# Performance work log

Measured on AMD Instinct MI355X. Metric: run time of the kernel, lower is better.

## Reference

```python
import jax, jax.numpy as jnp
import numpy as np

N = 50000
E = 800000
IN, HID, OUT = 256, 128, 64
NEG_SLOPE = 0.2


def _gat(x, src, dst, W, a_src, a_dst, b, heads, dim, concat):
    # PyG GATConv (eval mode, self-loops already appended to src/dst)
    xh = (x @ W).reshape(N, heads, dim)              # [N,H,D]
    s_src = jnp.einsum('nhd,hd->nh', xh, a_src)       # [N,H]
    s_dst = jnp.einsum('nhd,hd->nh', xh, a_dst)
    e = jax.nn.leaky_relu(s_src[src] + s_dst[dst], NEG_SLOPE)  # [Etot,H]
    m = jax.ops.segment_max(e, dst, num_segments=N)
    e = jnp.exp(e - m[dst])
    z = jax.ops.segment_sum(e, dst, num_segments=N)
    alpha = e / z[dst]                                # segment softmax over incoming edges
    msg = xh[src] * alpha[:, :, None]                 # [Etot,H,D] gather + weight
    out = jax.ops.segment_sum(msg, dst, num_segments=N)  # scatter-add aggregate
    out = out.reshape(N, heads * dim) if concat else out.mean(axis=1)
    return out + b


def setup_inputs():
    key = jax.random.key(0)
    ks = jax.random.split(key, 20)
    sc = 0.05
    inp = {
        'x': jax.random.normal(ks[0], (N, IN), jnp.float32),
        'edge_index': jax.random.randint(ks[1], (2, E), 0, N, jnp.int64) if jax.config.read('jax_enable_x64') else jax.random.randint(ks[1], (2, E), 0, N, jnp.int32),
        # semantic MLP
        'w1': jax.random.normal(ks[2], (IN, HID), jnp.float32) * sc,
        'b1': jnp.zeros((HID,), jnp.float32),
        'w2': jax.random.normal(ks[3], (HID, HID), jnp.float32) * sc,
        'b2': jnp.zeros((HID,), jnp.float32),
        # gat1: HID -> HID//2, heads=4, concat -> 2*HID
        'g1_w': jax.random.normal(ks[4], (HID, 4 * (HID // 2)), jnp.float32) * sc,
        'g1_asrc': jax.random.normal(ks[5], (4, HID // 2), jnp.float32) * sc,
        'g1_adst': jax.random.normal(ks[6], (4, HID // 2), jnp.float32) * sc,
        'g1_b': jnp.zeros((2 * HID,), jnp.float32),
        # gat2: 2*HID -> OUT, heads=2, mean
        'g2_w': jax.random.normal(ks[7], (2 * HID, 2 * OUT), jnp.float32) * sc,
        'g2_asrc': jax.random.normal(ks[8], (2, OUT), jnp.float32) * sc,
        'g2_adst': jax.random.normal(ks[9], (2, OUT), jnp.float32) * sc,
        'g2_b': jnp.zeros((OUT,), jnp.float32),
        # gat3: OUT -> OUT, heads=1, mean
        'g3_w': jax.random.normal(ks[10], (OUT, OUT), jnp.float32) * sc,
        'g3_asrc': jax.random.normal(ks[11], (1, OUT), jnp.float32) * sc,
        'g3_adst': jax.random.normal(ks[12], (1, OUT), jnp.float32) * sc,
        'g3_b': jnp.zeros((OUT,), jnp.float32),
    }
    return inp


def reference(x, edge_index, w1, b1, w2, b2,
              g1_w, g1_asrc, g1_adst, g1_b,
              g2_w, g2_asrc, g2_adst, g2_b,
              g3_w, g3_asrc, g3_adst, g3_b):
    # add self loops once (PyG GATConv default add_self_loops=True)
    loop = jnp.arange(N, dtype=edge_index.dtype)
    src = jnp.concatenate([edge_index[0], loop])
    dst = jnp.concatenate([edge_index[1], loop])
    # semantic MLP (eval: dropout is identity)
    h = jax.nn.relu(x @ w1 + b1)
    h = jax.nn.relu(h @ w2 + b2)
    h = jax.nn.elu(_gat(h, src, dst, g1_w, g1_asrc, g1_adst, g1_b, 4, HID // 2, True))
    h = jax.nn.elu(_gat(h, src, dst, g2_w, g2_asrc, g2_adst, g2_b, 2, OUT, False))
    h = _gat(h, src, dst, g3_w, g3_asrc, g3_adst, g3_b, 1, OUT, False)
    return h
```

## Files before the change

### kernel.cpp

```cpp
#include <hip/hip_runtime.h>
#include <hip/hip_fp16.h>
#include <math.h>

#define NN 50000
#define NE 800000

static inline int ceil_div_h(int a, int b) { return (a + b - 1) / b; }

typedef _Float16 half8 __attribute__((ext_vector_type(8)));
typedef float f32x4 __attribute__((ext_vector_type(4)));

__global__ __launch_bounds__(256)
void prep_kernel(const float* __restrict__ w1, const float* __restrict__ w2,
                 const float* __restrict__ g1w, const float* __restrict__ g2w,
                 const float* __restrict__ g3w, __half* __restrict__ wt,
                 int* __restrict__ cursor) {
  int idx = blockIdx.x * 256 + threadIdx.x;
  if (idx < NN) cursor[idx] = 0;
  const float* W; int K, N, li;
  if (idx < 32768)        { W = w1;  K = 256; N = 128; li = idx; }
  else if (idx < 49152)   { W = w2;  K = 128; N = 128; li = idx - 32768; }
  else if (idx < 81920)   { W = g1w; K = 128; N = 256; li = idx - 49152; }
  else if (idx < 114688)  { W = g2w; K = 256; N = 128; li = idx - 81920; }
  else if (idx < 118784)  { W = g3w; K = 64;  N = 64;  li = idx - 114688; }
  else return;
  int n = li / K, k = li - n * K;
  wt[idx] = __float2half_rn(W[(size_t)k * N + n]);
}

__global__ __launch_bounds__(256)
void mlp_gat1_fused(const float* __restrict__ x,
                    const __half* __restrict__ wt1,
                    const float* __restrict__ b1,
                    const __half* __restrict__ wt2,
                    const float* __restrict__ b2,
                    const __half* __restrict__ wtg1,
                    const float* __restrict__ a_src, const float* __restrict__ a_dst,
                    __half* __restrict__ xh1,
                    float* __restrict__ s_src, float* __restrict__ s_dst) {
  constexpr int SA = 40;
  constexpr int SH = 136;
  __shared__ __align__(16) _Float16 smem[25088];
  _Float16* As   = smem;
  _Float16* Bs12 = smem + 2560;
  _Float16* h1s  = smem + 7680;
  _Float16* h2s  = smem + 16384;
  _Float16* Bs3  = Bs12;
  const int tid = threadIdx.x;
  const int bm = blockIdx.x * 64;
  const int wave = tid >> 6, lane = tid & 63;
  const int l16 = lane & 15, quad = lane >> 4;
  const int wm = (wave & 1) * 32;
  const int wn = (wave >> 1) * 64;

  {
    f32x4 acc[2][4] = {};
    for (int k0 = 0; k0 < 256; k0 += 32) {
      #pragma unroll
      for (int i = 0; i < 2; ++i) {
        int idx = tid + i * 256;
        int m = idx >> 3, q = idx & 7;
        int gm = bm + m;
        float4 v = make_float4(0.f, 0.f, 0.f, 0.f);
        if (gm < NN) v = *(const float4*)&x[(size_t)gm * 256 + k0 + q * 4];
        union { __half2 h2[2]; float2 f2; } u;
        u.h2[0] = __floats2half2_rn(v.x, v.y);
        u.h2[1] = __floats2half2_rn(v.z, v.w);
        *(float2*)&As[m * SA + q * 4] = u.f2;
      }
      #pragma unroll
      for (int i = 0; i < 2; ++i) {
        int idx = tid + i * 256;
        int n = idx >> 2, kq = (idx & 3) * 8;
        *(float4*)&Bs12[n * SA + kq] = *(const float4*)&wt1[(size_t)n * 256 + k0 + kq];
      }
      __syncthreads();
      half8 af[2], bf[4];
      #pragma unroll
      for (int mi = 0; mi < 2; ++mi)
        af[mi] = *(const half8*)&As[(wm + mi * 16 + l16) * SA + quad * 8];
      #pragma unroll
      for (int ni = 0; ni < 4; ++ni)
        bf[ni] = *(const half8*)&Bs12[(wn + ni * 16 + l16) * SA + quad * 8];
      #pragma unroll
      for (int mi = 0; mi < 2; ++mi)
        #pragma unroll
        for (int ni = 0; ni < 4; ++ni)
          acc[mi][ni] = __builtin_amdgcn_mfma_f32_16x16x32_f16(af[mi], bf[ni], acc[mi][ni], 0, 0, 0);
      __syncthreads();
    }
    #pragma unroll
    for (int mi = 0; mi < 2; ++mi)
      #pragma unroll
      for (int r = 0; r < 4; ++r) {
        int row = wm + mi * 16 + quad * 4 + r;
        #pragma unroll
        for (int ni = 0; ni < 4; ++ni) {
          int col = wn + ni * 16 + l16;
          float v = acc[mi][ni][r] + b1[col];
          v = fmaxf(v, 0.f);
          h1s[row * SH + col] = (_Float16)v;
        }
      }
  }
  __syncthreads();

  {
    f32x4 acc[2][4] = {};
    for (int k0 = 0; k0 < 128; k0 += 32) {
      #pragma unroll
      for (int i = 0; i < 2; ++i) {
        int idx = tid + i * 256;
        int n = idx >> 2, kq = (idx & 3) * 8;
        *(float4*)&Bs12[n * SA + kq] = *(const float4*)&wt2[(size_t)n * 128 + k0 + kq];
      }
      __syncthreads();
      half8 af[2], bf[4];
      #pragma unroll
      for (int mi = 0; mi < 2; ++mi)
        af[mi] = *(const half8*)&h1s[(wm + mi * 16 + l16) * SH + k0 + quad * 8];
      #pragma unroll
      for (int ni = 0; ni < 4; ++ni)
        bf[ni] = *(const half8*)&Bs12[(wn + ni * 16 + l16) * SA + quad * 8];
      #pragma unroll
      for (int mi = 0; mi < 2; ++mi)
        #pragma unroll
        for (int ni = 0; ni < 4; ++ni)
          acc[mi][ni] = __builtin_amdgcn_mfma_f32_16x16x32_f16(af[mi], bf[ni], acc[mi][ni], 0, 0, 0);
      __syncthreads();
    }
    #pragma unroll
    for (int mi = 0; mi < 2; ++mi)
      #pragma unroll
      for (int r = 0; r < 4; ++r) {
        int row = wm + mi * 16 + quad * 4 + r;
        #pragma unroll
        for (int ni = 0; ni < 4; ++ni) {
          int col = wn + ni * 16 + l16;
          float v = acc[mi][ni][r] + b2[col];
          v = fmaxf(v, 0.f);
          h2s[row * SH + col] = (_Float16)v;
        }
      }
  }
  __syncthreads();

  {
    f32x4 acc[4][4] = {};
    const int wn3 = wave * 64;
    for (int k0 = 0; k0 < 128; k0 += 32) {
      #pragma unroll
      for (int i = 0; i < 4; ++i) {
        int idx = tid + i * 256;
        int n = idx >> 2, kq = (idx & 3) * 8;
        *(float4*)&Bs3[n * SA + kq] = *(const float4*)&wtg1[(size_t)n * 128 + k0 + kq];
      }
      __syncthreads();
      half8 af[4], bf[4];
      #pragma unroll
      for (int mi = 0; mi < 4; ++mi)
        af[mi] = *(const half8*)&h2s[(mi * 16 + l16) * SH + k0 + quad * 8];
      #pragma unroll
      for (int ni = 0; ni < 4; ++ni)
        bf[ni] = *(const half8*)&Bs3[(wn3 + ni * 16 + l16) * SA + quad * 8];
      #pragma unroll
      for (int mi = 0; mi < 4; ++mi)
        #pragma unroll
        for (int ni = 0; ni < 4; ++ni)
          acc[mi][ni] = __builtin_amdgcn_mfma_f32_16x16x32_f16(af[mi], bf[ni], acc[mi][ni], 0, 0, 0);
      __syncthreads();
    }
    float asv[4], adv[4];
    #pragma unroll
    for (int ni = 0; ni < 4; ++ni) {
      int d = ni * 16 + l16;
      asv[ni] = a_src[wave * 64 + d];
      adv[ni] = a_dst[wave * 64 + d];
    }
    #pragma unroll
    for (int mi = 0; mi < 4; ++mi) {
      #pragma unroll
      for (int r = 0; r < 4; ++r) {
        int gm = bm + mi * 16 + quad * 4 + r;
        float ss = 0.f, sd = 0.f;
        #pragma unroll
        for (int ni = 0; ni < 4; ++ni) {
          float v = acc[mi][ni][r];
          ss = fmaf(v, asv[ni], ss);
          sd = fmaf(v, adv[ni], sd);
          if (gm < NN) xh1[(size_t)gm * 256 + wn3 + ni * 16 + l16] = __float2half_rn(v);
        }
        #pragma unroll
        for (int off = 1; off < 16; off <<= 1) {
          ss += __shfl_xor(ss, off, 64);
          sd += __shfl_xor(sd, off, 64);
        }
        if (l16 == 0 && gm < NN) {
          s_src[gm * 4 + wave] = ss;
          s_dst[gm * 4 + wave] = sd;
        }
      }
    }
  }
}

template<int BM, int TN, int WR, int WC, int ACT, int OUTH, int AF32, int HS>
__global__ __launch_bounds__(256)
void mfma_gemm(const void* __restrict__ Av, const __half* __restrict__ Bt,
               const float* __restrict__ bias, void* __restrict__ Cv,
               const float* __restrict__ a_src, const float* __restrict__ a_dst,
               float* __restrict__ s_src, float* __restrict__ s_dst,
               int M, int N, int K) {
  constexpr int FM = BM / WR / 16;
  constexpr int FN = TN / WC / 16;
  constexpr int SA = 40;
  __shared__ __align__(16) _Float16 As[BM * SA];
  __shared__ __align__(16) _Float16 Bs[TN * SA];
  const int tid = threadIdx.x;
  const int bm = blockIdx.y * BM, bn = blockIdx.x * TN;
  const int wave = tid >> 6, lane = tid & 63;
  const int wm = (wave % WR) * (BM / WR);
  const int wn = (wave / WR) * (TN / WC);
  const int l16 = lane & 15, quad = lane >> 4;

  f32x4 acc[FM][FN] = {};

  for (int k0 = 0; k0 < K; k0 += 32) {
    if (AF32) {
      const float* A = (const float*)Av;
      #pragma unroll
      for (int i = 0; i < (BM * 8) / 256; ++i) {
        int idx = tid + i * 256;
        int m = idx >> 3, q = idx & 7;
        int gm = bm + m;
        float4 v = make_float4(0.f, 0.f, 0.f, 0.f);
        if (gm < M) v = *(const float4*)&A[(size_t)gm * K + k0 + q * 4];
        union { __half2 h2[2]; float2 f2; } u;
        u.h2[0] = __floats2half2_rn(v.x, v.y);
        u.h2[1] = __floats2half2_rn(v.z, v.w);
        *(float2*)&As[m * SA + q * 4] = u.f2;
      }
    } else {
      const __half* A = (const __half*)Av;
      #pragma unroll
      for (int i = 0; i < (BM * 4) / 256; ++i) {
        int idx = tid + i * 256;
        int m = idx >> 2, q = (idx & 3) * 8;
        int gm = bm + m;
        float4 raw = make_float4(0.f, 0.f, 0.f, 0.f);
        if (gm < M) raw = *(const float4*)&A[(size_t)gm * K + k0 + q];
        *(float4*)&As[m * SA + q] = raw;
      }
    }
    #pragma unroll
    for (int i = 0; i < (TN * 4) / 256; ++i) {
      int idx = tid + i * 256;
      int n = idx >> 2, kq = (idx & 3) * 8;
      float4 raw = *(const float4*)&Bt[(size_t)(bn + n) * K + k0 + kq];
      *(float4*)&Bs[n * SA + kq] = raw;
    }
    __syncthreads();
    half8 af[FM], bf[FN];
    #pragma unroll
    for (int mi = 0; mi < FM; ++mi)
      af[mi] = *(const half8*)&As[(wm + mi * 16 + l16) * SA + quad * 8];
    #pragma unroll
    for (int ni = 0; ni < FN; ++ni)
      bf[ni] = *(const half8*)&Bs[(wn + ni * 16 + l16) * SA + quad * 8];
    #pragma unroll
    for (int mi = 0; mi < FM; ++mi)
      #pragma unroll
      for (int ni = 0; ni < FN; ++ni)
        acc[mi][ni] = __builtin_amdgcn_mfma_f32_16x16x32_f16(af[mi], bf[ni], acc[mi][ni], 0, 0, 0);
    __syncthreads();
  }

  #pragma unroll
  for (int mi = 0; mi < FM; ++mi) {
    #pragma unroll
    for (int r = 0; r < 4; ++r) {
      int gm = bm + wm + mi * 16 + quad * 4 + r;
      if (gm >= M) continue;
      #pragma unroll
      for (int ni = 0; ni < FN; ++ni) {
        int gn = bn + wn + ni * 16 + l16;
        float v = acc[mi][ni][r];
        if (bias) v += bias[gn];
        if (ACT == 1) v = fmaxf(v, 0.f);
        if (OUTH) ((__half*)Cv)[(size_t)gm * N + gn] = __float2half_rn(v);
        else      ((float*)Cv)[(size_t)gm * N + gn] = v;
      }
    }
  }

  if (HS > 0) {
    const int h = (bn + wn) >> 6;
    float asv[FN], adv[FN];
    #pragma unroll
    for (int ni = 0; ni < FN; ++ni) {
      int d = ni * 16 + l16;
      asv[ni] = a_src[h * 64 + d];
      adv[ni] = a_dst[h * 64 + d];
    }
    #pragma unroll
    for (int mi = 0; mi < FM; ++mi) {
      #pragma unroll
      for (int r = 0; r < 4; ++r) {
        float ss = 0.f, sd = 0.f;
        #pragma unroll
        for (int ni = 0; ni < FN; ++ni) {
          float v = acc[mi][ni][r];
          ss = fmaf(v, asv[ni], ss);
          sd = fmaf(v, adv[ni], sd);
        }
        #pragma unroll
        for (int off = 1; off < 16; off <<= 1) {
          ss += __shfl_xor(ss, off, 64);
          sd += __shfl_xor(sd, off, 64);
        }
        int gm = bm + wm + mi * 16 + quad * 4 + r;
        if (l16 == 0 && gm < M) {
          s_src[gm * HS + h] = ss;
          s_dst[gm * HS + h] = sd;
        }
      }
    }
  }
}


__global__ __launch_bounds__(256)
void hist_kernel(const int* __restrict__ ei, int* __restrict__ cnt) {
  int e = blockIdx.x * blockDim.x + threadIdx.x;
  if (e >= NE) return;
  atomicAdd(&cnt[ei[NE + e]], 1);
}

__global__ __launch_bounds__(256)
void scan1_kernel(const int* __restrict__ in, int* __restrict__ out,
                  int* __restrict__ bsum, int n) {
  __shared__ int tmp[256];
  int t = threadIdx.x;
  int i = blockIdx.x * 256 + t;
  int v = (i < n) ? in[i] : 0;
  tmp[t] = v;
  __syncthreads();
  for (int off = 1; off < 256; off <<= 1) {
    int u = (t >= off) ? tmp[t - off] : 0;
    __syncthreads();
    tmp[t] += u;
    __syncthreads();
  }
  if (i <= n) out[i] = tmp[t] - v;
  if (t == 255) bsum[blockIdx.x] = tmp[255];
}

__global__ __launch_bounds__(256)
void scan3_kernel(int* __restrict__ out, const int* __restrict__ bsum,
                  int* __restrict__ cursor, int n, int nb) {
  __shared__ int tmp[256];
  int t = threadIdx.x;
  int bv = (t < nb) ? bsum[t] : 0;
  tmp[t] = bv;
  __syncthreads();
  for (int off = 1; off < 256; off <<= 1) {
    int u = (t >= off) ? tmp[t - off] : 0;
    __syncthreads();
    tmp[t] += u;
    __syncthreads();
  }
  int add = tmp[blockIdx.x] - ((blockIdx.x < nb) ? bsum[blockIdx.x] : 0);
  int i = blockIdx.x * 256 + t;
  if (i > n) return;
  int v = out[i] + add;
  out[i] = v;
  if (i < n) cursor[i] = v;
}

__global__ __launch_bounds__(256)
void scatter_kernel(const int* __restrict__ ei, int* __restrict__ cursor,
                    int* __restrict__ srcs) {
  int e = blockIdx.x * blockDim.x + threadIdx.x;
  if (e >= NE) return;
  int s = ei[e], d = ei[NE + e];
  int pos = atomicAdd(&cursor[d], 1);
  srcs[pos] = s;
}

template<int H, int MODE>
__global__ __launch_bounds__(256)
void gat_aggregate(const int* __restrict__ rowptr, const int* __restrict__ srcs,
                   const float* __restrict__ ssrc, const float* __restrict__ sdst,
                   const __half* __restrict__ xh, const float* __restrict__ bias,
                   void* __restrict__ outv) {
  constexpr int HD = H * 64;
  __shared__ float wbuf[4][64 * H];
  __shared__ int sbuf[4][64];
  const int wslot = threadIdx.x >> 6;
  const int wid = (blockIdx.x * blockDim.x + threadIdx.x) >> 6;
  const int lane = threadIdx.x & 63;
  if (wid >= NN) return;
  const int n = wid;
  const int start = rowptr[n];
  const int end = rowptr[n + 1];
  const int h = (lane * H) >> 6;

  float sdv[H];
  #pragma unroll
  for (int hh = 0; hh < H; ++hh) sdv[hh] = sdst[n * H + hh];

  float z;
  float acc[H];
  {
    float wself[H];
    #pragma unroll
    for (int hh = 0; hh < H; ++hh) {
      float e = ssrc[n * H + hh] + sdv[hh];
      e = e >= 0.f ? e : 0.2f * e;
      wself[hh] = __expf(e);
    }
    float ws = wself[h];
    z = ws;
    const __half* xr = xh + (size_t)n * HD + lane * H;
    if (H == 4) {
      float2 raw = *(const float2*)xr;
      __half2 p0 = *(__half2*)&raw.x;
      __half2 p1 = *(__half2*)&raw.y;
      float2 f0 = __half22float2(p0), f1 = __half22float2(p1);
      acc[0] = ws * f0.x; acc[1] = ws * f0.y; acc[2] = ws * f1.x; acc[3] = ws * f1.y;
    } else if (H == 2) {
      float2 f0 = __half22float2(*(const __half2*)xr);
      acc[0] = ws * f0.x; acc[1] = ws * f0.y;
    } else {
      acc[0] = ws * __half2float(xr[0]);
    }
  }

  for (int base = start; base < end; base += 64) {
    int cnt = end - base;
    if (cnt > 64) cnt = 64;
    if (lane < cnt) {
      int s = srcs[base + lane];
      sbuf[wslot][lane] = s;
      float ev[H];
      if (H == 4) {
        float4 t = *(const float4*)&ssrc[s * 4];
        ev[0] = t.x; ev[1] = t.y; ev[2] = t.z; ev[3] = t.w;
      } else if (H == 2) {
        float2 t = *(const float2*)&ssrc[s * 2];
        ev[0] = t.x; ev[1] = t.y;
      } else {
        ev[0] = ssrc[s];
      }
      #pragma unroll
      for (int hh = 0; hh < H; ++hh) {
        float e = ev[hh] + sdv[hh];
        e = e >= 0.f ? e : 0.2f * e;
        wbuf[wslot][lane * H + hh] = __expf(e);
      }
    }
    #pragma unroll 8
    for (int j = 0; j < cnt; ++j) {
      int s = sbuf[wslot][j];
      float w = wbuf[wslot][j * H + h];
      z += w;
      const __half* xr = xh + (size_t)s * HD + lane * H;
      if (H == 4) {
        float2 raw = *(const float2*)xr;
        __half2 p0 = *(__half2*)&raw.x;
        __half2 p1 = *(__half2*)&raw.y;
        float2 f0 = __half22float2(p0), f1 = __half22float2(p1);
        acc[0] = fmaf(w, f0.x, acc[0]); acc[1] = fmaf(w, f0.y, acc[1]);
        acc[2] = fmaf(w, f1.x, acc[2]); acc[3] = fmaf(w, f1.y, acc[3]);
      } else if (H == 2) {
        float2 f0 = __half22float2(*(const __half2*)xr);
        acc[0] = fmaf(w, f0.x, acc[0]); acc[1] = fmaf(w, f0.y, acc[1]);
      } else {
        acc[0] = fmaf(w, __half2float(xr[0]), acc[0]);
      }
    }
  }
  const float inv = 1.f / z;

  if (MODE == 0) {
    __half* out = (__half*)outv;
    float v[4];
    #pragma unroll
    for (int i = 0; i < 4; ++i) {
      v[i] = acc[i] * inv + bias[lane * 4 + i];
      v[i] = v[i] > 0.f ? v[i] : expm1f(v[i]);
    }
    union { __half2 h2[2]; float2 f2; } u;
    u.h2[0] = __floats2half2_rn(v[0], v[1]);
    u.h2[1] = __floats2half2_rn(v[2], v[3]);
    *(float2*)&out[(size_t)n * 256 + lane * 4] = u.f2;
  } else if (MODE == 1) {
    __half* out = (__half*)outv;
    float sv[2];
    #pragma unroll
    for (int i = 0; i < 2; ++i) {
      float mine = acc[i] * inv;
      float other = __shfl_xor(mine, 32, 64);
      sv[i] = (mine + other) * 0.5f;
    }
    if (lane < 32) {
      float v0 = sv[0] + bias[lane * 2 + 0];
      float v1 = sv[1] + bias[lane * 2 + 1];
      v0 = v0 > 0.f ? v0 : expm1f(v0);
      v1 = v1 > 0.f ? v1 : expm1f(v1);
      *(__half2*)&out[(size_t)n * 64 + lane * 2] = __floats2half2_rn(v0, v1);
    }
  } else {
    float* out = (float*)outv;
    out[(size_t)n * 64 + lane] = acc[0] * inv + bias[lane];
  }
}


extern "C" void kernel_launch(void* const* d_in, const int* in_sizes, int n_in,
                              void* d_out, int out_size, void* d_ws, size_t ws_size,
                              hipStream_t stream) {
  const float* x    = (const float*)d_in[0];
  const int*   ei   = (const int*)d_in[1];
  const float* w1   = (const float*)d_in[2];
  const float* b1   = (const float*)d_in[3];
  const float* w2   = (const float*)d_in[4];
  const float* b2   = (const float*)d_in[5];
  const float* g1w  = (const float*)d_in[6];
  const float* g1as = (const float*)d_in[7];
  const float* g1ad = (const float*)d_in[8];
  const float* g1b  = (const float*)d_in[9];
  const float* g2w  = (const float*)d_in[10];
  const float* g2as = (const float*)d_in[11];
  const float* g2ad = (const float*)d_in[12];
  const float* g2b  = (const float*)d_in[13];
  const float* g3w  = (const float*)d_in[14];
  const float* g3as = (const float*)d_in[15];
  const float* g3ad = (const float*)d_in[16];
  const float* g3b  = (const float*)d_in[17];
  float* out = (float*)d_out;

  float* ws   = (float*)d_ws;
  float* bufA = ws;
  float* bufB = bufA + (size_t)NN * 256;
  float* bufC = bufB + (size_t)NN * 256;
  float* ssrc = bufC + (size_t)NN * 256;
  float* sdst = ssrc + (size_t)NN * 4;
  int* rowptr = (int*)(sdst + (size_t)NN * 4);
  int* cursor = rowptr + (NN + 1);
  int* bsum   = cursor + NN;
  int* srcs   = bsum + 256;
  __half* wt   = (__half*)(srcs + NE);
  __half* wt1  = wt;
  __half* wt2  = wt + 32768;
  __half* wtg1 = wt + 49152;
  __half* wtg2 = wt + 81920;
  __half* wtg3 = wt + 114688;

  __half* xh1 = (__half*)bufC;
  __half* a1  = (__half*)bufA;
  __half* xh2 = (__half*)bufB;
  __half* a2  = (__half*)bufC;
  __half* xh3 = (__half*)bufB;

  const int TB = 256;
  const int grid_m = ceil_div_h(NN, 64);
  const int egrid = ceil_div_h(NE, TB);
  const int sgrid = ceil_div_h(NN + 1, TB);
  const int wgrid = ceil_div_h(NN, 4);

  prep_kernel<<<ceil_div_h(118784, TB), TB, 0, stream>>>(w1, w2, g1w, g2w, g3w, wt, cursor);

  hist_kernel<<<egrid, TB, 0, stream>>>(ei, cursor);
  scan1_kernel<<<sgrid, TB, 0, stream>>>(cursor, rowptr, bsum, NN);
  scan3_kernel<<<sgrid, TB, 0, stream>>>(rowptr, bsum, cursor, NN, sgrid);
  scatter_kernel<<<egrid, TB, 0, stream>>>(ei, cursor, srcs);

  mlp_gat1_fused<<<grid_m, TB, 0, stream>>>(x, wt1, b1, wt2, b2, wtg1,
                                            g1as, g1ad, xh1, ssrc, sdst);
  gat_aggregate<4, 0><<<wgrid, TB, 0, stream>>>(rowptr, srcs, ssrc, sdst, xh1, g1b, a1);

  mfma_gemm<64, 128, 2, 2, 0, 1, 0, 2><<<dim3(1, grid_m), TB, 0, stream>>>(
      a1, wtg2, nullptr, xh2, g2as, g2ad, ssrc, sdst, NN, 128, 256);
  gat_aggregate<2, 1><<<wgrid, TB, 0, stream>>>(rowptr, srcs, ssrc, sdst, xh2, g2b, a2);

  mfma_gemm<64, 64, 4, 1, 0, 1, 0, 1><<<dim3(1, grid_m), TB, 0, stream>>>(
      a2, wtg3, nullptr, xh3, g3as, g3ad, ssrc, sdst, NN, 64, 64);
  gat_aggregate<1, 2><<<wgrid, TB, 0, stream>>>(rowptr, srcs, ssrc, sdst, xh3, g3b, out);
}
```

Baseline: 408.9 us.

## Pack multiple nodes per wavefront in GAT2/GAT3 aggregation with 4-wide lanes

Specialises the 4-head aggregation into its own kernel, with the inner unroll reduced from 8 to 4. It adds a sub-wave kernel for the 2-head and 1-head layers in which each lane handles 4 features, so one wavefront processes 2 or 4 destination nodes at once. Per-edge attention weights are computed inline per lane instead of staged through shared memory. This aims to stop small-feature layers from leaving most lanes idle or issuing narrow loads, at the cost of redundant exp work per edge and more divergence from uneven node degrees within a wave.

```diff
diff --git a/kernel.cpp b/kernel.cpp
--- a/kernel.cpp
+++ b/kernel.cpp
@@ -387,13 +387,12 @@
   srcs[pos] = s;
 }
 
-template<int H, int MODE>
-__global__ __launch_bounds__(256)
-void gat_aggregate(const int* __restrict__ rowptr, const int* __restrict__ srcs,
-                   const float* __restrict__ ssrc, const float* __restrict__ sdst,
-                   const __half* __restrict__ xh, const float* __restrict__ bias,
-                   void* __restrict__ outv) {
-  constexpr int HD = H * 64;
+__global__ __launch_bounds__(256)
+void gat_aggregate4(const int* __restrict__ rowptr, const int* __restrict__ srcs,
+                    const float* __restrict__ ssrc, const float* __restrict__ sdst,
+                    const __half* __restrict__ xh, const float* __restrict__ bias,
+                    __half* __restrict__ out) {
+  constexpr int H = 4, HD = 256;
   __shared__ float wbuf[4][64 * H];
   __shared__ int sbuf[4][64];
   const int wslot = threadIdx.x >> 6;
@@ -403,7 +402,7 @@
   const int n = wid;
   const int start = rowptr[n];
   const int end = rowptr[n + 1];
-  const int h = (lane * H) >> 6;
+  const int h = lane >> 4;
 
   float sdv[H];
   #pragma unroll
@@ -422,18 +421,11 @@
     float ws = wself[h];
     z = ws;
     const __half* xr = xh + (size_t)n * HD + lane * H;
-    if (H == 4) {
-      float2 raw = *(const float2*)xr;
-      __half2 p0 = *(__half2*)&raw.x;
-      __half2 p1 = *(__half2*)&raw.y;
-      float2 f0 = __half22float2(p0), f1 = __half22float2(p1);
-      acc[0] = ws * f0.x; acc[1] = ws * f0.y; acc[2] = ws * f1.x; acc[3] = ws * f1.y;
-    } else if (H == 2) {
-      float2 f0 = __half22float2(*(const __half2*)xr);
-      acc[0] = ws * f0.x; acc[1] = ws * f0.y;
-    } else {
-      acc[0] = ws * __half2float(xr[0]);
-    }
+    float2 raw = *(const float2*)xr;
+    __half2 p0 = *(__half2*)&raw.x;
+    __half2 p1 = *(__half2*)&raw.y;
+    float2 f0 = __half22float2(p0), f1 = __half22float2(p1);
+    acc[0] = ws * f0.x; acc[1] = ws * f0.y; acc[2] = ws * f1.x; acc[3] = ws * f1.y;
   }
 
   for (int base = start; base < end; base += 64) {
@@ -442,16 +434,8 @@
     if (lane < cnt) {
       int s = srcs[base + lane];
       sbuf[wslot][lane] = s;
-      float ev[H];
-      if (H == 4) {
-        float4 t = *(const float4*)&ssrc[s * 4];
-        ev[0] = t.x; ev[1] = t.y; ev[2] = t.z; ev[3] = t.w;
-      } else if (H == 2) {
-        float2 t = *(const float2*)&ssrc[s * 2];
-        ev[0] = t.x; ev[1] = t.y;
-      } else {
-        ev[0] = ssrc[s];
-      }
+      float4 t = *(const float4*)&ssrc[s * 4];
+      float ev[H] = {t.x, t.y, t.z, t.w};
       #pragma unroll
       for (int hh = 0; hh < H; ++hh) {
         float e = ev[hh] + sdv[hh];
@@ -459,60 +443,118 @@
         wbuf[wslot][lane * H + hh] = __expf(e);
       }
     }
-    #pragma unroll 8
+    #pragma unroll 4
     for (int j = 0; j < cnt; ++j) {
       int s = sbuf[wslot][j];
       float w = wbuf[wslot][j * H + h];
       z += w;
       const __half* xr = xh + (size_t)s * HD + lane * H;
-      if (H == 4) {
-        float2 raw = *(const float2*)xr;
-        __half2 p0 = *(__half2*)&raw.x;
-        __half2 p1 = *(__half2*)&raw.y;
-        float2 f0 = __half22float2(p0), f1 = __half22float2(p1);
-        acc[0] = fmaf(w, f0.x, acc[0]); acc[1] = fmaf(w, f0.y, acc[1]);
-        acc[2] = fmaf(w, f1.x, acc[2]); acc[3] = fmaf(w, f1.y, acc[3]);
-      } else if (H == 2) {
-        float2 f0 = __half22float2(*(const __half2*)xr);
-        acc[0] = fmaf(w, f0.x, acc[0]); acc[1] = fmaf(w, f0.y, acc[1]);
-      } else {
-        acc[0] = fmaf(w, __half2float(xr[0]), acc[0]);
-      }
+      float2 raw = *(const float2*)xr;
+      __half2 p0 = *(__half2*)&raw.x;
+      __half2 p1 = *(__half2*)&raw.y;
+      float2 f0 = __half22float2(p0), f1 = __half22float2(p1);
+      acc[0] = fmaf(w, f0.x, acc[0]); acc[1] = fmaf(w, f0.y, acc[1]);
+      acc[2] = fmaf(w, f1.x, acc[2]); acc[3] = fmaf(w, f1.y, acc[3]);
     }
   }
   const float inv = 1.f / z;
 
-  if (MODE == 0) {
-    __half* out = (__half*)outv;
-    float v[4];
-    #pragma unroll
-    for (int i = 0; i < 4; ++i) {
-      v[i] = acc[i] * inv + bias[lane * 4 + i];
-      v[i] = v[i] > 0.f ? v[i] : expm1f(v[i]);
-    }
-    union { __half2 h2[2]; float2 f2; } u;
-    u.h2[0] = __floats2half2_rn(v[0], v[1]);
-    u.h2[1] = __floats2half2_rn(v[2], v[3]);
-    *(float2*)&out[(size_t)n * 256 + lane * 4] = u.f2;
-  } else if (MODE == 1) {
-    __half* out = (__half*)outv;
-    float sv[2];
-    #pragma unroll
-    for (int i = 0; i < 2; ++i) {
-      float mine = acc[i] * inv;
-      float other = __shfl_xor(mine, 32, 64);
-      sv[i] = (mine + other) * 0.5f;
-    }
-    if (lane < 32) {
-      float v0 = sv[0] + bias[lane * 2 + 0];
-      float v1 = sv[1] + bias[lane * 2 + 1];
-      v0 = v0 > 0.f ? v0 : expm1f(v0);
-      v1 = v1 > 0.f ? v1 : expm1f(v1);
-      *(__half2*)&out[(size_t)n * 64 + lane * 2] = __floats2half2_rn(v0, v1);
+  float v[4];
+  #pragma unroll
+  for (int i = 0; i < 4; ++i) {
+    v[i] = acc[i] * inv + bias[lane * 4 + i];
+    v[i] = v[i] > 0.f ? v[i] : expm1f(v[i]);
+  }
+  union { __half2 h2[2]; float2 f2; } u;
+  u.h2[0] = __floats2half2_rn(v[0], v[1]);
+  u.h2[1] = __floats2half2_rn(v[2], v[3]);
+  *(float2*)&out[(size_t)n * 256 + lane * 4] = u.f2;
+}
+
+template<int H, int MODE>
+__global__ __launch_bounds__(256)
+void gat_aggregate_sub(const int* __restrict__ rowptr, const int* __restrict__ srcs,
+                       const float* __restrict__ ssrc, const float* __restrict__ sdst,
+                       const __half* __restrict__ xh, const float* __restrict__ bias,
+                       void* __restrict__ outv) {
+  constexpr int HD   = H * 64;
+  constexpr int GL   = HD / 4;
+  constexpr int NSUB = 64 / GL;
+  const int wid  = (blockIdx.x * blockDim.x + threadIdx.x) >> 6;
+  const int lane = threadIdx.x & 63;
+  const int sg = lane / GL;
+  const int p  = lane - sg * GL;
+  const int n  = wid * NSUB + sg;
+  const int hp = (p * 4) >> 6;
+  const bool alive = (n < NN);
+
+  int start = 0, end = 0;
+  float sdv = 0.f;
+  if (alive) {
+    start = rowptr[n];
+    end = rowptr[n + 1];
+    sdv = sdst[n * H + hp];
+  }
+
+  float z = 0.f;
+  float a0 = 0.f, a1 = 0.f, a2 = 0.f, a3 = 0.f;
+
+  if (alive) {
+    float e = ssrc[n * H + hp] + sdv;
+    e = e >= 0.f ? e : 0.2f * e;
+    float w = __expf(e);
+    z = w;
+    float2 raw = *(const float2*)(xh + (size_t)n * HD + p * 4);
+    __half2 p0 = *(__half2*)&raw.x, p1 = *(__half2*)&raw.y;
+    float2 f0 = __half22float2(p0), f1 = __half22float2(p1);
+    a0 = w * f0.x; a1 = w * f0.y; a2 = w * f1.x; a3 = w * f1.y;
+  }
+
+  for (int j = start; j < end; ++j) {
+    int s = srcs[j];
+    float e = ssrc[s * H + hp] + sdv;
+    e = e >= 0.f ? e : 0.2f * e;
+    float w = __expf(e);
+    z += w;
+    float2 raw = *(const float2*)(xh + (size_t)s * HD + p * 4);
+    __half2 p0 = *(__half2*)&raw.x, p1 = *(__half2*)&raw.y;
+    float2 f0 = __half22float2(p0), f1 = __half22float2(p1);
+    a0 = fmaf(w, f0.x, a0); a1 = fmaf(w, f0.y, a1);
+    a2 = fmaf(w, f1.x, a2); a3 = fmaf(w, f1.y, a3);
+  }
+
+  const float inv = 1.f / z;
+
+  if (MODE == 1) {
+    float v0 = a0 * inv, v1 = a1 * inv, v2 = a2 * inv, v3 = a3 * inv;
+    float o0 = __shfl_xor(v0, 16, 64);
+    float o1 = __shfl_xor(v1, 16, 64);
+    float o2 = __shfl_xor(v2, 16, 64);
+    float o3 = __shfl_xor(v3, 16, 64);
+    if (alive && hp == 0) {
+      float m0 = (v0 + o0) * 0.5f + bias[p * 4 + 0];
+      float m1 = (v1 + o1) * 0.5f + bias[p * 4 + 1];
+      float m2 = (v2 + o2) * 0.5f + bias[p * 4 + 2];
+      float m3 = (v3 + o3) * 0.5f + bias[p * 4 + 3];
+      m0 = m0 > 0.f ? m0 : expm1f(m0);
+      m1 = m1 > 0.f ? m1 : expm1f(m1);
+      m2 = m2 > 0.f ? m2 : expm1f(m2);
+      m3 = m3 > 0.f ? m3 : expm1f(m3);
+      __half* out = (__half*)outv;
+      union { __half2 h2[2]; float2 f2; } u;
+      u.h2[0] = __floats2half2_rn(m0, m1);
+      u.h2[1] = __floats2half2_rn(m2, m3);
+      *(float2*)&out[(size_t)n * 64 + p * 4] = u.f2;
     }
   } else {
-    float* out = (float*)outv;
-    out[(size_t)n * 64 + lane] = acc[0] * inv + bias[lane];
+    if (alive) {
+      float* out = (float*)outv;
+      float4 o = make_float4(a0 * inv + bias[p * 4 + 0],
+                             a1 * inv + bias[p * 4 + 1],
+                             a2 * inv + bias[p * 4 + 2],
+                             a3 * inv + bias[p * 4 + 3]);
+      *(float4*)&out[(size_t)n * 64 + p * 4] = o;
+    }
   }
 }
 
@@ -578,13 +620,15 @@
 
   mlp_gat1_fused<<<grid_m, TB, 0, stream>>>(x, wt1, b1, wt2, b2, wtg1,
                                             g1as, g1ad, xh1, ssrc, sdst);
-  gat_aggregate<4, 0><<<wgrid, TB, 0, stream>>>(rowptr, srcs, ssrc, sdst, xh1, g1b, a1);
+  gat_aggregate4<<<wgrid, TB, 0, stream>>>(rowptr, srcs, ssrc, sdst, xh1, g1b, a1);
 
   mfma_gemm<64, 128, 2, 2, 0, 1, 0, 2><<<dim3(1, grid_m), TB, 0, stream>>>(
       a1, wtg2, nullptr, xh2, g2as, g2ad, ssrc, sdst, NN, 128, 256);
-  gat_aggregate<2, 1><<<wgrid, TB, 0, stream>>>(rowptr, srcs, ssrc, sdst, xh2, g2b, a2);
+  gat_aggregate_sub<2, 1><<<ceil_div_h(NN, 8), TB, 0, stream>>>(
+      rowptr, srcs, ssrc, sdst, xh2, g2b, a2);
 
   mfma_gemm<64, 64, 4, 1, 0, 1, 0, 1><<<dim3(1, grid_m), TB, 0, stream>>>(
       a2, wtg3, nullptr, xh3, g3as, g3ad, ssrc, sdst, NN, 64, 64);
-  gat_aggregate<1, 2><<<wgrid, TB, 0, stream>>>(rowptr, srcs, ssrc, sdst, xh3, g3b, out);
-}
+  gat_aggregate_sub<1, 2><<<ceil_div_h(NN, 16), TB, 0, stream>>>(
+      rowptr, srcs, ssrc, sdst, xh3, g3b, out);
+}
```

Measured after the change: 431.0 us. 1.05x slower.
